# Performance work log

Measured on AMD Instinct MI355X. Metric: run time of the kernel, lower is better.

Reference implementation:

```python
import jax, jax.numpy as jnp
import numpy as np
from functools import partial

N_Q = 4
SEQ = 4096
EMB = 512
VOCAB = 50257
TAGS = 64

def _qlayer(ang, p):
    """4-qubit circuit: RY(ang_i) encoding on |0>, RX(p_i) per wire, CNOT chain, <Z_i>.
    ang, p: (4,) float32. Returns (4,) float32 Pauli-Z expectations."""
    c, s = jnp.cos(ang * 0.5), jnp.sin(ang * 0.5)
    q = jnp.stack([c, s], axis=-1).astype(jnp.complex64)  # (4,2) per-qubit state after RY
    cp, sp = jnp.cos(p * 0.5), jnp.sin(p * 0.5)
    # RX(p) = [[cos, -i sin],[-i sin, cos]] applied per wire (still a product state)
    a0 = cp * q[:, 0] - 1j * sp * q[:, 1]
    a1 = -1j * sp * q[:, 0] + cp * q[:, 1]
    q = jnp.stack([a0, a1], axis=-1)  # (4,2)
    # full 16-dim statevector as tensor (2,2,2,2), dim i = wire i
    st = jnp.einsum('a,b,c,d->abcd', q[0], q[1], q[2], q[3])
    # CNOT chain: control wire i, target wire i+1
    for i in range(N_Q - 1):
        st0, st1 = jnp.split(st, 2, axis=i)        # control = 0 / 1
        st1 = jnp.flip(st1, axis=i + 1)            # flip target where control = 1
        st = jnp.concatenate([st0, st1], axis=i)
    probs = st.real ** 2 + st.imag ** 2            # (2,2,2,2)
    zs = []
    for i in range(N_Q):
        pi = jnp.sum(probs, axis=tuple(j for j in range(N_Q) if j != i))  # (2,)
        zs.append(pi[0] - pi[1])
    return jnp.stack(zs)  # (4,)


def setup_inputs() -> dict:
    key = jax.random.key(0)
    ks = jax.random.split(key, 16)
    d_in = EMB + N_Q
    sc = 1.0 / np.sqrt(d_in)
    inp = {
        'sentence': jax.random.randint(ks[0], (SEQ,), 0, VOCAB),
        'emb': jax.random.normal(ks[1], (VOCAB, EMB), jnp.float32),
        'Wf': jax.random.normal(ks[2], (d_in, N_Q), jnp.float32) * sc,
        'bf': jnp.zeros((N_Q,), jnp.float32),
        'Wi': jax.random.normal(ks[3], (d_in, N_Q), jnp.float32) * sc,
        'bi': jnp.zeros((N_Q,), jnp.float32),
        'Wu': jax.random.normal(ks[4], (d_in, N_Q), jnp.float32) * sc,
        'bu': jnp.zeros((N_Q,), jnp.float32),
        'Wo': jax.random.normal(ks[5], (d_in, N_Q), jnp.float32) * sc,
        'bo': jnp.zeros((N_Q,), jnp.float32),
        'qf': jax.random.normal(ks[6], (N_Q,), jnp.float32),
        'qi': jax.random.normal(ks[7], (N_Q,), jnp.float32),
        'qu': jax.random.normal(ks[8], (N_Q,), jnp.float32),
        'qo': jax.random.normal(ks[9], (N_Q,), jnp.float32),
        'W_tag': jax.random.normal(ks[10], (N_Q, TAGS), jnp.float32) * 0.5,
        'b_tag': jnp.zeros((TAGS,), jnp.float32),
    }
    return inp


def reference(sentence, emb, Wf, bf, Wi, bi, Wu, bu, Wo, bo, qf, qi, qu, qo, W_tag, b_tag):
    embeds = emb[sentence]  # (S, E)

    def step(carry, x):
        hx, cx = carry
        comb = jnp.concatenate([x, hx])  # (E+4,)
        f = jax.nn.sigmoid(_qlayer(comb @ Wf + bf, qf))
        i = jax.nn.sigmoid(_qlayer(comb @ Wi + bi, qi))
        g = jnp.tanh(_qlayer(comb @ Wu + bu, qu))
        o = jax.nn.sigmoid(_qlayer(comb @ Wo + bo, qo))
        cx = f * cx + i * g
        hx = o * jnp.tanh(cx)
        return (hx, cx), hx

    h0 = jnp.zeros((N_Q,), jnp.float32)
    _, hs = jax.lax.scan(step, (h0, h0), embeds)  # hs: (S, 4)
    logits = hs @ W_tag + b_tag                    # (S, TAGS)
    return jax.nn.log_softmax(logits, axis=1)
```

## Files before the change

kernel.cpp:

```cpp
#include <hip/hip_runtime.h>
#include <hip/hip_bf16.h>

#define N_Q    4
#define SEQ    4096
#define EMB    512
#define TAGS   64
#define INV2PI 0.15915494309189535f
#define CHUNK  32
#define WARM   32
#define NCHUNK (SEQ / CHUNK)

#define WS_WT 0
#define WS_BB 8192
#define WS_XP 8208
#define WS_HS 73808

#define DPPF(OLD, SRC, CTRL, RM, BM) \
  __int_as_float(__builtin_amdgcn_update_dpp(__float_as_int(OLD), __float_as_int(SRC), (CTRL), (RM), (BM), false))

__global__ __launch_bounds__(256) void k0_wt(
    const float* __restrict__ Wf, const float* __restrict__ Wi,
    const float* __restrict__ Wu, const float* __restrict__ Wo,
    const float* __restrict__ bf, const float* __restrict__ bi,
    const float* __restrict__ bu, const float* __restrict__ bo,
    float* __restrict__ WT, float* __restrict__ bb)
{
  int tid = blockIdx.x * blockDim.x + threadIdx.x;
  int c = tid >> 9;
  int e = tid & 511;
  int g = c >> 2, k = c & 3;
  const float* W = (g == 0) ? Wf : (g == 1) ? Wi : (g == 2) ? Wu : Wo;
  WT[c * EMB + e] = W[e * 4 + k] * INV2PI;
  if (tid < 16) {
    int g2 = tid >> 2, k2 = tid & 3;
    const float* b = (g2 == 0) ? bf : (g2 == 1) ? bi : (g2 == 2) ? bu : bo;
    bb[tid] = b[k2] * INV2PI;
  }
}

__global__ __launch_bounds__(256) void k1_xp(
    const int* __restrict__ sent, const float* __restrict__ emb,
    const float* __restrict__ WT, const float* __restrict__ bb,
    float* __restrict__ xp)
{
  int idx = blockIdx.x * 256 + threadIdx.x;
  int t = idx >> 4;
  int c = idx & 15;
  const float4* x = (const float4*)(emb + (size_t)sent[t] * EMB);
  const float4* w = (const float4*)(WT + c * EMB);
  float a0 = 0.f, a1 = 0.f, a2 = 0.f, a3 = 0.f;
#pragma unroll 8
  for (int e4 = 0; e4 < EMB / 4; ++e4) {
    float4 xv = x[e4];
    float4 wv = w[e4];
    a0 = fmaf(xv.x, wv.x, a0);
    a1 = fmaf(xv.y, wv.y, a1);
    a2 = fmaf(xv.z, wv.z, a2);
    a3 = fmaf(xv.w, wv.w, a3);
  }
  float dot = (a0 + a1) + (a2 + a3) + bb[c];
  int p = ((c & 3) << 2) | (c >> 2);
  xp[t * 16 + p] = dot;
}

__global__ __launch_bounds__(64) void k2_rec(
    const float* __restrict__ xp,
    const float* __restrict__ Wf, const float* __restrict__ Wi,
    const float* __restrict__ Wu, const float* __restrict__ Wo,
    const float* __restrict__ qf, const float* __restrict__ qi,
    const float* __restrict__ qu, const float* __restrict__ qo,
    float* __restrict__ hs)
{
  const int lane = threadIdx.x & 63;
  const int p = lane & 15;
  const int k = p >> 2;
  const int g = p & 3;
  const float* W = (g == 0) ? Wf : (g == 1) ? Wi : (g == 2) ? Wu : Wo;
  const float* q = (g == 0) ? qf : (g == 1) ? qi : (g == 2) ? qu : qo;

  float wh0 = W[(EMB + 0) * 4 + k] * INV2PI;
  float wh1 = W[(EMB + 1) * 4 + k] * INV2PI;
  float wh2 = W[(EMB + 2) * 4 + k] * INV2PI;
  float wh3 = W[(EMB + 3) * 4 + k] * INV2PI;

  int s1i = __builtin_amdgcn_update_dpp(k, k, 0x124, 0xF, 0xF, false);
  int s2i = __builtin_amdgcn_update_dpp(k, k, 0x128, 0xF, 0xF, false);
  int s3i = __builtin_amdgcn_update_dpp(k, k, 0x12C, 0xF, 0xF, false);
  #define SELW(KK) ((KK) == 0 ? wh0 : (KK) == 1 ? wh1 : (KK) == 2 ? wh2 : wh3)
  float W0 = SELW(k);
  float W1 = SELW(s1i);
  float W2 = SELW(s2i);
  float W3 = SELW(s3i);

  float cc0 = cosf(q[0]);
  float cc1 = cc0 * cosf(q[1]);
  float cc2 = cc1 * cosf(q[2]);
  float cc3 = cc2 * cosf(q[3]);
  float cq = (k == 0) ? cc0 : (k == 1) ? cc1 : (k == 2) ? cc2 : cc3;

  float P0, P1, P2, P3, D;
  if (g == 2) {
    P0 = 0.99990143f; P1 = -0.33104735f; P2 = 0.12044012f; P3 = -0.02770000f; D = 0.0f;
  } else {
    P0 = 0.25f; P1 = -0.020833334f; P2 = 0.0020833334f; P3 = -2.1081349e-4f; D = 0.5f;
  }
  float cq2 = cq * cq;
  float K0c = P0 * cq;
  float K1c = P1 * cq * cq2;
  float K2c = P2 * cq * cq2 * cq2;
  float K3c = P3 * cq * cq2 * cq2 * cq2;

  int c_id = blockIdx.x;
  int t_real = c_id * CHUNK;
  int t0 = t_real - WARM; if (t0 < 0) t0 = 0;
  int t_end = t_real + CHUNK;

  const float* base = xp + p;
  float xb0 = base[t0 * 16];
  float xb1 = base[(t0 + 1) * 16];
  float xb2 = base[(t0 + 2) * 16];

  float hx = 0.f, cx = 0.f;
  const float one = 1.0f;

  for (int t = t0; t < t_end; ++t) {
    float xpv = xb0; xb0 = xb1; xb1 = xb2;
    xb2 = base[(t + 3) * 16];

    float r1 = DPPF(hx, hx, 0x124, 0xF, 0xF);
    float r2 = DPPF(hx, hx, 0x128, 0xF, 0xF);
    float r3 = DPPF(hx, hx, 0x12C, 0xF, 0xF);
    float A1 = fmaf(hx, W0, xpv);
    float B1 = r1 * W1;
    float A2 = fmaf(r2, W2, A1);
    float B2 = fmaf(r3, W3, B1);
    float ang = A2 + B2;

    float cv = __builtin_amdgcn_cosf(ang);

    float sA = DPPF(one, cv, 0x114, 0xF, 0xE);
    float m1 = cv * sA;
    float sB = DPPF(one, m1, 0x118, 0xF, 0xC);
    float m  = m1 * sB;

    float y = m * m;
    float pp = fmaf(y, K3c, K2c);
    pp = fmaf(y, pp, K1c);
    pp = fmaf(y, pp, K0c);
    float v = fmaf(m, pp, D);

    float vf = DPPF(v, v, 0x00, 0xF, 0xF);
    float vi = DPPF(v, v, 0x55, 0xF, 0xF);
    float vu = DPPF(v, v, 0xAA, 0xF, 0xF);
    float vo = DPPF(v, v, 0xFF, 0xF, 0xF);

    cx = fmaf(vf, cx, vi * vu);

    float e2 = __builtin_amdgcn_exp2f(2.885390082f * cx);
    float rr = __builtin_amdgcn_rcpf(e2 + 1.0f);
    hx = fmaf(-2.0f * vo, rr, vo);

    if (t >= t_real) hs[t * 4 + k] = hx;
  }
}

__global__ __launch_bounds__(256) void k3_out(
    const float* __restrict__ hs, const float* __restrict__ Wt,
    const float* __restrict__ bt, float* __restrict__ out)
{
  int t = blockIdx.x * 4 + (threadIdx.x >> 6);
  int j = threadIdx.x & 63;
  float4 h = *(const float4*)(hs + t * 4);
  float z = bt[j];
  z = fmaf(h.x, Wt[j],       z);
  z = fmaf(h.y, Wt[64 + j],  z);
  z = fmaf(h.z, Wt[128 + j], z);
  z = fmaf(h.w, Wt[192 + j], z);
  float e = __builtin_amdgcn_exp2f(z * 1.4426950408889634f);
  float s = e;
#pragma unroll
  for (int off = 32; off > 0; off >>= 1) s += __shfl_xor(s, off, 64);
  out[t * 64 + j] = z - __builtin_amdgcn_logf(s) * 0.69314718055994531f;
}

extern "C" void kernel_launch(void* const* d_in, const int* in_sizes, int n_in,
                              void* d_out, int out_size, void* d_ws, size_t ws_size,
                              hipStream_t stream) {
  (void)in_sizes; (void)n_in; (void)out_size; (void)ws_size;
  const int*   sent = (const int*)  d_in[0];
  const float* emb  = (const float*)d_in[1];
  const float* Wf   = (const float*)d_in[2];
  const float* bf   = (const float*)d_in[3];
  const float* Wi   = (const float*)d_in[4];
  const float* bi   = (const float*)d_in[5];
  const float* Wu   = (const float*)d_in[6];
  const float* bu   = (const float*)d_in[7];
  const float* Wo   = (const float*)d_in[8];
  const float* bo   = (const float*)d_in[9];
  const float* qf   = (const float*)d_in[10];
  const float* qi   = (const float*)d_in[11];
  const float* qu   = (const float*)d_in[12];
  const float* qo   = (const float*)d_in[13];
  const float* Wt   = (const float*)d_in[14];
  const float* bt   = (const float*)d_in[15];

  float* ws = (float*)d_ws;
  float* WT = ws + WS_WT;
  float* bb = ws + WS_BB;
  float* xp = ws + WS_XP;
  float* hs = ws + WS_HS;
  float* out = (float*)d_out;

  k0_wt<<<dim3(32),   dim3(256), 0, stream>>>(Wf, Wi, Wu, Wo, bf, bi, bu, bo, WT, bb);
  k1_xp<<<dim3(256),  dim3(256), 0, stream>>>(sent, emb, WT, bb, xp);
  k2_rec<<<dim3(NCHUNK), dim3(64), 0, stream>>>(xp, Wf, Wi, Wu, Wo, qf, qi, qu, qo, hs);
  k3_out<<<dim3(1024), dim3(256), 0, stream>>>(hs, Wt, bt, out);
}
```

Measured before the change: 194.3 us.

## Fuse weight transpose into projection and output head into recurrence kernel

Removes the separate weight-transpose kernel: each projection block now stages transposed gate weights in shared memory and applies the 1/2π scale after the dot product. The tag projection and log-softmax are fused into the recurrence kernel through a per-chunk shared-memory buffer, which eliminates the hs round trip and a launch. Chunk size is halved and warm-up shortened to double the number of parallel recurrence blocks. The cost is that every projection block redundantly loads the full weight set, and the shorter warm-up may lose accuracy.

```diff
diff --git a/kernel.cpp b/kernel.cpp
--- a/kernel.cpp
+++ b/kernel.cpp
@@ -6,48 +6,45 @@
 #define EMB    512
 #define TAGS   64
 #define INV2PI 0.15915494309189535f
-#define CHUNK  32
-#define WARM   32
+#define CHUNK  16
+#define WARM   24
 #define NCHUNK (SEQ / CHUNK)
 
-#define WS_WT 0
-#define WS_BB 8192
-#define WS_XP 8208
-#define WS_HS 73808
+#define WS_XP 0
 
 #define DPPF(OLD, SRC, CTRL, RM, BM) \
   __int_as_float(__builtin_amdgcn_update_dpp(__float_as_int(OLD), __float_as_int(SRC), (CTRL), (RM), (BM), false))
 
-__global__ __launch_bounds__(256) void k0_wt(
+__global__ __launch_bounds__(256) void k1_xp(
+    const int* __restrict__ sent, const float* __restrict__ emb,
     const float* __restrict__ Wf, const float* __restrict__ Wi,
     const float* __restrict__ Wu, const float* __restrict__ Wo,
     const float* __restrict__ bf, const float* __restrict__ bi,
     const float* __restrict__ bu, const float* __restrict__ bo,
-    float* __restrict__ WT, float* __restrict__ bb)
-{
-  int tid = blockIdx.x * blockDim.x + threadIdx.x;
-  int c = tid >> 9;
-  int e = tid & 511;
-  int g = c >> 2, k = c & 3;
-  const float* W = (g == 0) ? Wf : (g == 1) ? Wi : (g == 2) ? Wu : Wo;
-  WT[c * EMB + e] = W[e * 4 + k] * INV2PI;
-  if (tid < 16) {
-    int g2 = tid >> 2, k2 = tid & 3;
-    const float* b = (g2 == 0) ? bf : (g2 == 1) ? bi : (g2 == 2) ? bu : bo;
-    bb[tid] = b[k2] * INV2PI;
-  }
-}
-
-__global__ __launch_bounds__(256) void k1_xp(
-    const int* __restrict__ sent, const float* __restrict__ emb,
-    const float* __restrict__ WT, const float* __restrict__ bb,
     float* __restrict__ xp)
 {
-  int idx = blockIdx.x * 256 + threadIdx.x;
-  int t = idx >> 4;
-  int c = idx & 15;
+  __shared__ float colbuf[16 * 516];
+  int tid = threadIdx.x;
+#pragma unroll
+  for (int g = 0; g < 4; ++g) {
+    const float* W = (g == 0) ? Wf : (g == 1) ? Wi : (g == 2) ? Wu : Wo;
+#pragma unroll
+    for (int half = 0; half < 2; ++half) {
+      int e = tid + half * 256;
+      float4 r = *(const float4*)(W + e * 4);
+      colbuf[(g * 4 + 0) * 516 + e] = r.x;
+      colbuf[(g * 4 + 1) * 516 + e] = r.y;
+      colbuf[(g * 4 + 2) * 516 + e] = r.z;
+      colbuf[(g * 4 + 3) * 516 + e] = r.w;
+    }
+  }
+  __syncthreads();
+
+  int t = blockIdx.x * 16 + (tid >> 4);
+  int c = tid & 15;
+  int g = c >> 2, k = c & 3;
   const float4* x = (const float4*)(emb + (size_t)sent[t] * EMB);
-  const float4* w = (const float4*)(WT + c * EMB);
+  const float4* w = (const float4*)(&colbuf[c * 516]);
   float a0 = 0.f, a1 = 0.f, a2 = 0.f, a3 = 0.f;
 #pragma unroll 8
   for (int e4 = 0; e4 < EMB / 4; ++e4) {
@@ -58,7 +55,8 @@
     a2 = fmaf(xv.z, wv.z, a2);
     a3 = fmaf(xv.w, wv.w, a3);
   }
-  float dot = (a0 + a1) + (a2 + a3) + bb[c];
+  const float* b = (g == 0) ? bf : (g == 1) ? bi : (g == 2) ? bu : bo;
+  float dot = ((a0 + a1) + (a2 + a3) + b[k]) * INV2PI;
   int p = ((c & 3) << 2) | (c >> 2);
   xp[t * 16 + p] = dot;
 }
@@ -69,14 +67,19 @@
     const float* __restrict__ Wu, const float* __restrict__ Wo,
     const float* __restrict__ qf, const float* __restrict__ qi,
     const float* __restrict__ qu, const float* __restrict__ qo,
-    float* __restrict__ hs)
+    const float* __restrict__ Wt, const float* __restrict__ bt,
+    float* __restrict__ out)
 {
+  __shared__ float hsh[CHUNK * 4];
   const int lane = threadIdx.x & 63;
   const int p = lane & 15;
   const int k = p >> 2;
   const int g = p & 3;
   const float* W = (g == 0) ? Wf : (g == 1) ? Wi : (g == 2) ? Wu : Wo;
   const float* q = (g == 0) ? qf : (g == 1) ? qi : (g == 2) ? qu : qo;
+
+  float wt0 = Wt[lane], wt1 = Wt[64 + lane], wt2 = Wt[128 + lane], wt3 = Wt[192 + lane];
+  float bj = bt[lane];
 
   float wh0 = W[(EMB + 0) * 4 + k] * INV2PI;
   float wh1 = W[(EMB + 1) * 4 + k] * INV2PI;
@@ -160,27 +163,26 @@
     float rr = __builtin_amdgcn_rcpf(e2 + 1.0f);
     hx = fmaf(-2.0f * vo, rr, vo);
 
-    if (t >= t_real) hs[t * 4 + k] = hx;
-  }
-}
-
-__global__ __launch_bounds__(256) void k3_out(
-    const float* __restrict__ hs, const float* __restrict__ Wt,
-    const float* __restrict__ bt, float* __restrict__ out)
-{
-  int t = blockIdx.x * 4 + (threadIdx.x >> 6);
-  int j = threadIdx.x & 63;
-  float4 h = *(const float4*)(hs + t * 4);
-  float z = bt[j];
-  z = fmaf(h.x, Wt[j],       z);
-  z = fmaf(h.y, Wt[64 + j],  z);
-  z = fmaf(h.z, Wt[128 + j], z);
-  z = fmaf(h.w, Wt[192 + j], z);
-  float e = __builtin_amdgcn_exp2f(z * 1.4426950408889634f);
-  float s = e;
-#pragma unroll
-  for (int off = 32; off > 0; off >>= 1) s += __shfl_xor(s, off, 64);
-  out[t * 64 + j] = z - __builtin_amdgcn_logf(s) * 0.69314718055994531f;
+    if (t >= t_real && lane < 16 && g == 0)
+      hsh[(t - t_real) * 4 + k] = hx;
+  }
+
+  __syncthreads();
+
+  float* orow = out + (size_t)t_real * 64 + lane;
+#pragma unroll
+  for (int dt = 0; dt < CHUNK; ++dt) {
+    float4 h = *(const float4*)(&hsh[dt * 4]);
+    float z = bj;
+    z = fmaf(h.x, wt0, z);
+    z = fmaf(h.y, wt1, z);
+    z = fmaf(h.z, wt2, z);
+    z = fmaf(h.w, wt3, z);
+    float s = __builtin_amdgcn_exp2f(z * 1.4426950408889634f);
+#pragma unroll
+    for (int off = 32; off > 0; off >>= 1) s += __shfl_xor(s, off, 64);
+    orow[dt * 64] = z - __builtin_amdgcn_logf(s) * 0.69314718055994531f;
+  }
 }
 
 extern "C" void kernel_launch(void* const* d_in, const int* in_sizes, int n_in,
@@ -204,15 +206,11 @@
   const float* Wt   = (const float*)d_in[14];
   const float* bt   = (const float*)d_in[15];
 
-  float* ws = (float*)d_ws;
-  float* WT = ws + WS_WT;
-  float* bb = ws + WS_BB;
-  float* xp = ws + WS_XP;
-  float* hs = ws + WS_HS;
+  float* xp  = (float*)d_ws + WS_XP;
   float* out = (float*)d_out;
 
-  k0_wt<<<dim3(32),   dim3(256), 0, stream>>>(Wf, Wi, Wu, Wo, bf, bi, bu, bo, WT, bb);
-  k1_xp<<<dim3(256),  dim3(256), 0, stream>>>(sent, emb, WT, bb, xp);
-  k2_rec<<<dim3(NCHUNK), dim3(64), 0, stream>>>(xp, Wf, Wi, Wu, Wo, qf, qi, qu, qo, hs);
-  k3_out<<<dim3(1024), dim3(256), 0, stream>>>(hs, Wt, bt, out);
+  k1_xp<<<dim3(256),  dim3(256), 0, stream>>>(sent, emb, Wf, Wi, Wu, Wo,
+                                              bf, bi, bu, bo, xp);
+  k2_rec<<<dim3(NCHUNK), dim3(64), 0, stream>>>(xp, Wf, Wi, Wu, Wo,
+                                                qf, qi, qu, qo, Wt, bt, out);
 }
```

After: 180.8 us. 7.0% less time.
